# Optimization experiments

Measured on AMD Instinct MI355X. Metric: run time of the kernel, lower is better.

## Reference

```python
import jax, jax.numpy as jnp
import numpy as np

NUM_HEADS = 16
INPUT_DIM = 1024  # == dim == qkv_scale


def setup_inputs() -> dict:
    key = jax.random.key(0)
    k1, k2, k3 = jax.random.split(key, 3)
    x = jax.random.normal(k1, (4, 2048, INPUT_DIM), dtype=jnp.float32)
    # torch Linear(input_dim, 3*dim): y = x @ W.T + b; we store W pre-transposed as [in, out]
    W_qkv = jax.random.normal(k2, (INPUT_DIM, 3 * INPUT_DIM), dtype=jnp.float32) * (INPUT_DIM ** -0.5)
    b_qkv = jax.random.normal(k3, (3 * INPUT_DIM,), dtype=jnp.float32) * 0.01
    return {"x": x, "W_qkv": W_qkv, "b_qkv": b_qkv}


def reference(x, W_qkv, b_qkv):
    b, n, _ = x.shape
    h = NUM_HEADS
    d = INPUT_DIM // h
    scale = INPUT_DIM ** 0.5  # qkv_scale**0.5, MULTIPLIED (no softmax, no division)

    qkv = x @ W_qkv + b_qkv                      # [b, n, 3*dim]
    # rearrange 'b n (h d k) -> k b h n d': last axis splits (h, d, 3), k fastest
    qkv = qkv.reshape(b, n, h, d, 3)
    q = jnp.transpose(qkv[..., 0], (0, 2, 1, 3))  # [b, h, n, d]
    k_ = jnp.transpose(qkv[..., 1], (0, 2, 1, 3))
    v = jnp.transpose(qkv[..., 2], (0, 2, 1, 3))

    attn = jnp.einsum('bhid,bhjd->bhij', q, k_) * scale  # [b, h, n, n]
    out = jnp.einsum('bhij,bhjd->bhid', attn, v)         # [b, h, n, d]
    return out
```

## Files before the change

### kernel.cpp

```cpp
#include <hip/hip_runtime.h>
#include <stdint.h>

#define DEV __device__ __forceinline__

typedef float f32x4 __attribute__((ext_vector_type(4)));
typedef __bf16 bf16x8 __attribute__((ext_vector_type(8)));
typedef short short8 __attribute__((ext_vector_type(8)));
typedef short short4v __attribute__((ext_vector_type(4)));

DEV unsigned short f2bf(float f) {
    union { float f; unsigned u; } c; c.f = f;
    unsigned u = c.u;
    u += 0x7fffu + ((u >> 16) & 1u);
    return (unsigned short)(u >> 16);
}
DEV void async_ld16(const void* g, void* l) {
    __builtin_amdgcn_global_load_lds(
        (const __attribute__((address_space(1))) unsigned int*)g,
        (__attribute__((address_space(3))) unsigned int*)l, 16, 0, 0);
}
DEV f32x4 mfma16(bf16x8 a, bf16x8 b, f32x4 c) {
    return __builtin_amdgcn_mfma_f32_16x16x32_bf16(a, b, c, 0, 0, 0);
}

__global__ __launch_bounds__(256) void k_prep(const float* __restrict__ x,
                                              const float* __restrict__ W,
                                              unsigned short* __restrict__ xb,
                                              unsigned short* __restrict__ Wt) {
    __shared__ float T[64][65];
    const int blk = blockIdx.x, t = threadIdx.x;
    if (blk < 4096) {
        int i = blk * 256 + t;
        const float4* xp = (const float4*)x;
        float4 a = xp[i * 2], b = xp[i * 2 + 1];
        short8 o;
        o[0] = (short)f2bf(a.x); o[1] = (short)f2bf(a.y);
        o[2] = (short)f2bf(a.z); o[3] = (short)f2bf(a.w);
        o[4] = (short)f2bf(b.x); o[5] = (short)f2bf(b.y);
        o[6] = (short)f2bf(b.z); o[7] = (short)f2bf(b.w);
        *(short8*)(xb + i * 8) = o;
    } else {
        int bx = blk - 4096;
        int k0 = (bx / 48) * 64, n0 = (bx % 48) * 64;
        int rr = t >> 4, c4 = (t & 15) * 4;
        for (int i = 0; i < 4; i++) {
            int row = rr + i * 16;
            float4 v = *(const float4*)(W + (unsigned)(k0 + row) * 3072u + n0 + c4);
            T[row][c4] = v.x; T[row][c4 + 1] = v.y; T[row][c4 + 2] = v.z; T[row][c4 + 3] = v.w;
        }
        __syncthreads();
        for (int i = 0; i < 4; i++) {
            int ncol = rr + i * 16;
            int n = n0 + ncol;
            int which = n % 3;
            int oc = (n / 192) * 64 + (n % 192) / 3;
            short4v o;
            o[0] = (short)f2bf(T[c4 + 0][ncol]);
            o[1] = (short)f2bf(T[c4 + 1][ncol]);
            o[2] = (short)f2bf(T[c4 + 2][ncol]);
            o[3] = (short)f2bf(T[c4 + 3][ncol]);
            *(short4v*)(Wt + (unsigned)which * 1048576u + (unsigned)oc * 1024u + k0 + c4) = o;
        }
    }
}

#define BARRIER() asm volatile("s_barrier" ::: "memory")
#define WAITV(n) do { asm volatile("s_waitcnt vmcnt(" #n ")" ::: "memory"); \
                      __builtin_amdgcn_sched_barrier(0); } while (0)

__global__ __launch_bounds__(512, 2) void k_qkv(const unsigned short* __restrict__ xb,
                                                const unsigned short* __restrict__ Wt,
                                                const float* __restrict__ bias,
                                                unsigned short* __restrict__ Qs,
                                                unsigned short* __restrict__ K,
                                                unsigned short* __restrict__ V) {
    __shared__ __align__(16) unsigned short As[3][256 * 64];
    __shared__ __align__(16) unsigned short Bs[3][128 * 64];

    const int o = blockIdx.x + 24 * blockIdx.y;
    const int w = (o & 7) * 96 + (o >> 3);
    const int mt = w / 24, nt = w % 24;
    const int m0 = mt * 256;
    const int plane = nt >> 3;
    const int pc0 = (nt & 7) * 128;
    const unsigned short* Xp = xb + (unsigned)m0 * 1024u;
    const unsigned short* Wp = Wt + (unsigned)plane * 1048576u + (unsigned)pc0 * 1024u;

    const int t = threadIdx.x;
    const int wave = t >> 6, lane = t & 63;
    const int lan15 = lane & 15, quad = lane >> 4;
    const int srow = t >> 3;
    const int schunk = t & 7;

    const bool swp = (plane == 0);
    const int ga = swp ? (wave & 1) : (wave >> 1);
    const int gb = swp ? (wave >> 1) : (wave & 1);

    f32x4 acc[4][4] = {};

#define STAGE(kt, b) do {                                                     \
        const int kk_ = (kt) * 64;                                            \
        _Pragma("unroll")                                                     \
        for (int i_ = 0; i_ < 4; i_++) {                                      \
            int r_ = i_ * 64 + srow;                                          \
            int c_ = schunk ^ (r_ & 7);                                       \
            async_ld16(Xp + (unsigned)r_ * 1024u + kk_ + c_ * 8,              \
                       (void*)(As[b] + (i_ * 64 + wave * 8) * 64));           \
        }                                                                     \
        _Pragma("unroll")                                                     \
        for (int i_ = 0; i_ < 2; i_++) {                                      \
            int r_ = i_ * 64 + srow;                                          \
            int c_ = schunk ^ (r_ & 7);                                       \
            async_ld16(Wp + (unsigned)r_ * 1024u + kk_ + c_ * 8,              \
                       (void*)(Bs[b] + (i_ * 64 + wave * 8) * 64));           \
        }                                                                     \
    } while (0)

    STAGE(0, 0);
    STAGE(1, 1);

    for (int kt = 0; kt < 16; kt++) {
        const int buf = kt % 3;
        if (kt + 2 < 16) {
            STAGE(kt + 2, (kt + 2) % 3);
            WAITV(12);
        } else if (kt + 1 < 16) {
            WAITV(6);
        } else {
            WAITV(0);
        }
        BARRIER();

        const unsigned short* Ab = (swp ? Bs[buf] : As[buf]) + ga * 64 * 64;
        const unsigned short* Bb = (swp ? As[buf] : Bs[buf]) + gb * 64 * 64;
#pragma unroll
        for (int ks = 0; ks < 2; ks++) {
            const int c0 = ks * 4 + quad;
            bf16x8 af[4], bfr[4];
#pragma unroll
            for (int tm = 0; tm < 4; tm++) {
                int row = tm * 16 + lan15;
                af[tm] = *(const bf16x8*)(Ab + row * 64 + (c0 ^ (row & 7)) * 8);
            }
#pragma unroll
            for (int tn = 0; tn < 4; tn++) {
                int row = tn * 16 + lan15;
                bfr[tn] = *(const bf16x8*)(Bb + row * 64 + (c0 ^ (row & 7)) * 8);
            }
            __builtin_amdgcn_s_setprio(1);
#pragma unroll
            for (int tm = 0; tm < 4; tm++)
#pragma unroll
                for (int tn = 0; tn < 4; tn++)
                    acc[tm][tn] = mfma16(af[tm], bfr[tn], acc[tm][tn]);
            __builtin_amdgcn_s_setprio(0);
        }
        BARRIER();
    }
#undef STAGE

    if (plane == 0) {
        const int cg = (wave & 1) * 64, tg = (wave >> 1) * 64;
#pragma unroll
        for (int tm = 0; tm < 4; tm++) {
            int c4 = pc0 + cg + tm * 16 + quad * 4;
            int h = c4 >> 6, dd = c4 & 63;
            float b0 = bias[h * 192 + (dd + 0) * 3];
            float b1 = bias[h * 192 + (dd + 1) * 3];
            float b2 = bias[h * 192 + (dd + 2) * 3];
            float b3 = bias[h * 192 + (dd + 3) * 3];
#pragma unroll
            for (int tn = 0; tn < 4; tn++) {
                int token = m0 + tg + tn * 16 + lan15;
                unsigned bb = (unsigned)(token >> 11), tl = (unsigned)(token & 2047);
                uint2 p;
                p.x = (unsigned)f2bf((acc[tm][tn][0] + b0) * 32.0f) |
                      ((unsigned)f2bf((acc[tm][tn][1] + b1) * 32.0f) << 16);
                p.y = (unsigned)f2bf((acc[tm][tn][2] + b2) * 32.0f) |
                      ((unsigned)f2bf((acc[tm][tn][3] + b3) * 32.0f) << 16);
                *(uint2*)(Qs + bb * 2097152u + tl * 1024u + c4) = p;
            }
        }
    } else {
        unsigned short* dst = (plane == 1) ? K : V;
        const int tg = (wave >> 1) * 64, cg = (wave & 1) * 64;
        const int batch = m0 >> 11;
#pragma unroll
        for (int tn = 0; tn < 4; tn++) {
            int cip = pc0 + cg + tn * 16 + lan15;
            int h = cip >> 6, d = cip & 63;
            float bv = bias[h * 192 + d * 3 + plane];
            unsigned kv_base = ((unsigned)(batch * 16 + h) * 64u + (unsigned)d) * 2048u;
#pragma unroll
            for (int tm = 0; tm < 4; tm++) {
                unsigned token0 = (unsigned)((m0 + tg + tm * 16 + quad * 4) & 2047);
                uint2 p;
                p.x = (unsigned)f2bf(acc[tm][tn][0] + bv) |
                      ((unsigned)f2bf(acc[tm][tn][1] + bv) << 16);
                p.y = (unsigned)f2bf(acc[tm][tn][2] + bv) |
                      ((unsigned)f2bf(acc[tm][tn][3] + bv) << 16);
                *(uint2*)(dst + kv_base + token0) = p;
            }
        }
    }
}

__global__ __launch_bounds__(256) void k_attn4(const unsigned short* __restrict__ Kt,
                                               const unsigned short* __restrict__ Vt,
                                               const unsigned short* __restrict__ Qs,
                                               float* __restrict__ out) {
    __shared__ __align__(16) unsigned short Ks[64 * 128];
    __shared__ __align__(16) unsigned short Vs[64 * 128];
    __shared__ __align__(16) unsigned short Msb[64 * 64];
    const int bh = blockIdx.x & 63, sub = blockIdx.x >> 6;
    const int b = bh >> 4, h = bh & 15;
    const int wave = threadIdx.x >> 6, lane = threadIdx.x & 63;
    const int lan15 = lane & 15, quad = lane >> 4;
    const unsigned base = (unsigned)bh * 131072u;
    const int mt0 = (wave & 1) * 2, nt0 = (wave >> 1) * 2;
    const int slr = wave * 16 + (lane >> 4), scs = lane & 15;

    f32x4 macc[2][2] = {};
    for (int j = 0; j < 16; j++) {
        __syncthreads();
        for (int i = 0; i < 4; i++) {
            int lr = slr + i * 4;
            int c = scs ^ (lr & 15);
            async_ld16(Kt + base + (unsigned)lr * 2048u + j * 128 + c * 8,
                       (void*)(Ks + (wave * 16 + i * 4) * 128));
            async_ld16(Vt + base + (unsigned)lr * 2048u + j * 128 + c * 8,
                       (void*)(Vs + (wave * 16 + i * 4) * 128));
        }
        __syncthreads();
        for (int ks2 = 0; ks2 < 4; ks2++) {
            int c0 = ks2 * 4 + quad;
            bf16x8 ak[2], bv[2];
            for (int i = 0; i < 2; i++) {
                int row = (mt0 + i) * 16 + lan15;
                ak[i] = *(const bf16x8*)(Ks + row * 128 + (c0 ^ (row & 15)) * 8);
            }
            for (int i = 0; i < 2; i++) {
                int row = (nt0 + i) * 16 + lan15;
                bv[i] = *(const bf16x8*)(Vs + row * 128 + (c0 ^ (row & 15)) * 8);
            }
            for (int i = 0; i < 2; i++)
                for (int j2 = 0; j2 < 2; j2++)
                    macc[i][j2] = mfma16(ak[i], bv[j2], macc[i][j2]);
        }
    }
    for (int i = 0; i < 2; i++)
        for (int j2 = 0; j2 < 2; j2++) {
            int d2 = (nt0 + j2) * 16 + lan15;
            int c4 = ((mt0 + i) * 4 + quad) ^ (d2 & 15);
            uint2 p;
            p.x = (unsigned)f2bf(macc[i][j2][0]) | ((unsigned)f2bf(macc[i][j2][1]) << 16);
            p.y = (unsigned)f2bf(macc[i][j2][2]) | ((unsigned)f2bf(macc[i][j2][3]) << 16);
            *(uint2*)(Msb + d2 * 64 + c4 * 4) = p;
        }
    __syncthreads();

    const int t0 = sub * 256 + wave * 64;
    f32x4 oacc[4][4] = {};
#pragma unroll
    for (int ks = 0; ks < 2; ks++) {
        bf16x8 af[4], bfr[4];
        for (int mt = 0; mt < 4; mt++) {
            int tok = t0 + mt * 16 + lan15;
            af[mt] = *(const bf16x8*)(Qs + (unsigned)b * 2097152u + (unsigned)tok * 1024u +
                                      h * 64 + ks * 32 + quad * 8);
        }
        for (int nt = 0; nt < 4; nt++) {
            int d2 = nt * 16 + lan15;
            int cA = ks * 8 + quad * 2;
            uint2 u0 = *(const uint2*)(Msb + d2 * 64 + ((cA) ^ (d2 & 15)) * 4);
            uint2 u1 = *(const uint2*)(Msb + d2 * 64 + ((cA + 1) ^ (d2 & 15)) * 4);
            union { uint4 u; bf16x8 v; } cv;
            cv.u.x = u0.x; cv.u.y = u0.y; cv.u.z = u1.x; cv.u.w = u1.y;
            bfr[nt] = cv.v;
        }
        for (int mt = 0; mt < 4; mt++)
            for (int nt = 0; nt < 4; nt++)
                oacc[mt][nt] = mfma16(af[mt], bfr[nt], oacc[mt][nt]);
    }
    for (int mt = 0; mt < 4; mt++)
        for (int nt = 0; nt < 4; nt++)
            for (int r = 0; r < 4; r++)
                out[base + (unsigned)(t0 + mt * 16 + quad * 4 + r) * 64u + nt * 16 + lan15] =
                    oacc[mt][nt][r];
}

extern "C" void kernel_launch(void* const* d_in, const int* in_sizes, int n_in,
                              void* d_out, int out_size, void* d_ws, size_t ws_size,
                              hipStream_t stream) {
    const float* x = (const float*)d_in[0];
    const float* W = (const float*)d_in[1];
    const float* b = (const float*)d_in[2];
    float* out = (float*)d_out;

    unsigned short* xb = (unsigned short*)d_ws;
    unsigned short* Wt = xb + 8388608;
    unsigned short* Qs = Wt + 3145728;
    unsigned short* Kt = Qs + 8388608;
    unsigned short* Vt = Kt + 8388608;

    k_prep<<<4864, 256, 0, stream>>>(x, W, xb, Wt);
    k_qkv<<<dim3(24, 32), 512, 0, stream>>>(xb, Wt, b, Qs, Kt, Vt);
    k_attn4<<<512, 256, 0, stream>>>(Kt, Vt, Qs, out);
}
```

Before: 190.3 us.

## Shrink QKV GEMM tile to 128x128 with double buffering and 256 threads

The QKV projection GEMM moves from 256x128 tiles with 512 threads and a three-stage LDS pipeline to 128x128 tiles with 256 threads and two-stage double buffering, launched as 1536 blocks with a remapped block-to-tile swizzle. It also drops the s_setprio hints around the MFMA loop. Smaller tiles mean more blocks and less LDS per block, which could raise occupancy and balance work across CUs. The cost is lower data reuse per block, more global traffic, and a shallower prefetch that may expose load latency.

```diff
diff --git a/kernel.cpp b/kernel.cpp
--- a/kernel.cpp
+++ b/kernel.cpp
@@ -68,19 +68,19 @@
 #define WAITV(n) do { asm volatile("s_waitcnt vmcnt(" #n ")" ::: "memory"); \
                       __builtin_amdgcn_sched_barrier(0); } while (0)
 
-__global__ __launch_bounds__(512, 2) void k_qkv(const unsigned short* __restrict__ xb,
+__global__ __launch_bounds__(256, 2) void k_qkv(const unsigned short* __restrict__ xb,
                                                 const unsigned short* __restrict__ Wt,
                                                 const float* __restrict__ bias,
                                                 unsigned short* __restrict__ Qs,
                                                 unsigned short* __restrict__ K,
                                                 unsigned short* __restrict__ V) {
-    __shared__ __align__(16) unsigned short As[3][256 * 64];
-    __shared__ __align__(16) unsigned short Bs[3][128 * 64];
-
-    const int o = blockIdx.x + 24 * blockIdx.y;
-    const int w = (o & 7) * 96 + (o >> 3);
+    __shared__ __align__(16) unsigned short As[2][128 * 64];
+    __shared__ __align__(16) unsigned short Bs[2][128 * 64];
+
+    const int o = blockIdx.x;
+    const int w = (o & 7) * 192 + (o >> 3);
     const int mt = w / 24, nt = w % 24;
-    const int m0 = mt * 256;
+    const int m0 = mt * 128;
     const int plane = nt >> 3;
     const int pc0 = (nt & 7) * 128;
     const unsigned short* Xp = xb + (unsigned)m0 * 1024u;
@@ -89,12 +89,12 @@
     const int t = threadIdx.x;
     const int wave = t >> 6, lane = t & 63;
     const int lan15 = lane & 15, quad = lane >> 4;
-    const int srow = t >> 3;
-    const int schunk = t & 7;
+    const int slr = wave * 32 + (lane >> 3);
+    const int scs = lane & 7;
 
     const bool swp = (plane == 0);
-    const int ga = swp ? (wave & 1) : (wave >> 1);
-    const int gb = swp ? (wave >> 1) : (wave & 1);
+    const int aw = (wave & 1) * 64;
+    const int bw = (wave >> 1) * 64;
 
     f32x4 acc[4][4] = {};
 
@@ -102,37 +102,29 @@
         const int kk_ = (kt) * 64;                                            \
         _Pragma("unroll")                                                     \
         for (int i_ = 0; i_ < 4; i_++) {                                      \
-            int r_ = i_ * 64 + srow;                                          \
-            int c_ = schunk ^ (r_ & 7);                                       \
+            int r_ = slr + i_ * 8;                                            \
+            int c_ = scs ^ (r_ & 7);                                          \
             async_ld16(Xp + (unsigned)r_ * 1024u + kk_ + c_ * 8,              \
-                       (void*)(As[b] + (i_ * 64 + wave * 8) * 64));           \
-        }                                                                     \
-        _Pragma("unroll")                                                     \
-        for (int i_ = 0; i_ < 2; i_++) {                                      \
-            int r_ = i_ * 64 + srow;                                          \
-            int c_ = schunk ^ (r_ & 7);                                       \
+                       (void*)(As[b] + (wave * 32 + i_ * 8) * 64));           \
             async_ld16(Wp + (unsigned)r_ * 1024u + kk_ + c_ * 8,              \
-                       (void*)(Bs[b] + (i_ * 64 + wave * 8) * 64));           \
+                       (void*)(Bs[b] + (wave * 32 + i_ * 8) * 64));           \
         }                                                                     \
     } while (0)
 
     STAGE(0, 0);
-    STAGE(1, 1);
 
     for (int kt = 0; kt < 16; kt++) {
-        const int buf = kt % 3;
-        if (kt + 2 < 16) {
-            STAGE(kt + 2, (kt + 2) % 3);
-            WAITV(12);
-        } else if (kt + 1 < 16) {
-            WAITV(6);
+        const int buf = kt & 1;
+        if (kt + 1 < 16) {
+            STAGE(kt + 1, buf ^ 1);
+            WAITV(8);
         } else {
             WAITV(0);
         }
         BARRIER();
 
-        const unsigned short* Ab = (swp ? Bs[buf] : As[buf]) + ga * 64 * 64;
-        const unsigned short* Bb = (swp ? As[buf] : Bs[buf]) + gb * 64 * 64;
+        const unsigned short* Ab = (swp ? Bs[buf] : As[buf]) + aw * 64;
+        const unsigned short* Bb = (swp ? As[buf] : Bs[buf]) + bw * 64;
 #pragma unroll
         for (int ks = 0; ks < 2; ks++) {
             const int c0 = ks * 4 + quad;
@@ -147,23 +139,20 @@
                 int row = tn * 16 + lan15;
                 bfr[tn] = *(const bf16x8*)(Bb + row * 64 + (c0 ^ (row & 7)) * 8);
             }
-            __builtin_amdgcn_s_setprio(1);
 #pragma unroll
             for (int tm = 0; tm < 4; tm++)
 #pragma unroll
                 for (int tn = 0; tn < 4; tn++)
                     acc[tm][tn] = mfma16(af[tm], bfr[tn], acc[tm][tn]);
-            __builtin_amdgcn_s_setprio(0);
         }
         BARRIER();
     }
 #undef STAGE
 
     if (plane == 0) {
-        const int cg = (wave & 1) * 64, tg = (wave >> 1) * 64;
 #pragma unroll
         for (int tm = 0; tm < 4; tm++) {
-            int c4 = pc0 + cg + tm * 16 + quad * 4;
+            int c4 = pc0 + aw + tm * 16 + quad * 4;
             int h = c4 >> 6, dd = c4 & 63;
             float b0 = bias[h * 192 + (dd + 0) * 3];
             float b1 = bias[h * 192 + (dd + 1) * 3];
@@ -171,7 +160,7 @@
             float b3 = bias[h * 192 + (dd + 3) * 3];
 #pragma unroll
             for (int tn = 0; tn < 4; tn++) {
-                int token = m0 + tg + tn * 16 + lan15;
+                int token = m0 + bw + tn * 16 + lan15;
                 unsigned bb = (unsigned)(token >> 11), tl = (unsigned)(token & 2047);
                 uint2 p;
                 p.x = (unsigned)f2bf((acc[tm][tn][0] + b0) * 32.0f) |
@@ -183,17 +172,16 @@
         }
     } else {
         unsigned short* dst = (plane == 1) ? K : V;
-        const int tg = (wave >> 1) * 64, cg = (wave & 1) * 64;
         const int batch = m0 >> 11;
 #pragma unroll
         for (int tn = 0; tn < 4; tn++) {
-            int cip = pc0 + cg + tn * 16 + lan15;
+            int cip = pc0 + bw + tn * 16 + lan15;
             int h = cip >> 6, d = cip & 63;
             float bv = bias[h * 192 + d * 3 + plane];
             unsigned kv_base = ((unsigned)(batch * 16 + h) * 64u + (unsigned)d) * 2048u;
 #pragma unroll
             for (int tm = 0; tm < 4; tm++) {
-                unsigned token0 = (unsigned)((m0 + tg + tm * 16 + quad * 4) & 2047);
+                unsigned token0 = (unsigned)((m0 + aw + tm * 16 + quad * 4) & 2047);
                 uint2 p;
                 p.x = (unsigned)f2bf(acc[tm][tn][0] + bv) |
                       ((unsigned)f2bf(acc[tm][tn][1] + bv) << 16);
@@ -304,6 +292,6 @@
     unsigned short* Vt = Kt + 8388608;
 
     k_prep<<<4864, 256, 0, stream>>>(x, W, xb, Wt);
-    k_qkv<<<dim3(24, 32), 512, 0, stream>>>(xb, Wt, b, Qs, Kt, Vt);
+    k_qkv<<<1536, 256, 0, stream>>>(xb, Wt, b, Qs, Kt, Vt);
     k_attn4<<<512, 256, 0, stream>>>(Kt, Vt, Qs, out);
 }
```

Result: faster. 182.0 us (-4.4%).
